# Optimization experiments

Hardware: AMD Instinct MI355X
Metric: run time of the kernel (lower is better)

Reference implementation:

```python
import jax, jax.numpy as jnp
import numpy as np

# Static configuration (matches init_kwargs)
B, C, H, W = 8, 64, 256, 256
WS = 8            # window size
HEADS = 4
DH = 16           # dim per head, HEADS*DH == C
L = WS * WS       # tokens per window
EPS_LN = 1e-5

# --- Swin relative-position index (static, numpy) ---
_coords = np.stack(np.meshgrid(np.arange(WS), np.arange(WS), indexing='ij'))  # [2,ws,ws]
_flat = _coords.reshape(2, -1)                                                # [2,L]
_rel = (_flat[:, :, None] - _flat[:, None, :]).transpose(1, 2, 0).copy()      # [L,L,2]
_rel[..., 0] += WS - 1
_rel[..., 1] += WS - 1
_rel[..., 0] *= 2 * WS - 1
REL_IDX = _rel.sum(-1)  # [L,L] ints in [0, (2ws-1)^2)


def _biasfree_ln(x, w):
    # x: [B,C,H,W]; BiasFree_LayerNorm over channel dim (biased var, no mean subtraction in scale)
    var = jnp.var(x, axis=1, keepdims=True)
    return x * jax.lax.rsqrt(var + EPS_LN) * w[None, :, None, None]


def _win_partition(t):  # [B,H,W,C] -> [N, L, C]
    t = t.reshape(B, H // WS, WS, W // WS, WS, C).transpose(0, 1, 3, 2, 4, 5)
    return t.reshape(-1, L, C)


def _win_reverse(t):  # [N, L, C] -> [B,H,W,C]
    t = t.reshape(B, H // WS, W // WS, WS, WS, C).transpose(0, 1, 3, 2, 4, 5)
    return t.reshape(B, H, W, C)


def _l2norm(t):
    # torch F.normalize(dim=-1) semantics
    n = jnp.sqrt(jnp.sum(t * t, axis=-1, keepdims=True))
    return t / jnp.maximum(n, 1e-12)


def _forward(x, illu_fea, ln1_w, ln2_w, w_qkv, b_qkv, rpb_table, w_proj, b_proj,
             temperature, w_qkv_m, w_dw, w_out_m):
    # ---------- spatial (window) attention branch ----------
    xs = _biasfree_ln(x, ln1_w).transpose(0, 2, 3, 1)          # [B,H,W,C]
    xw = _win_partition(xs)                                     # [N,L,C]
    iw = _win_partition(illu_fea.transpose(0, 2, 3, 1))         # [N,L,C]
    iw = iw.reshape(-1, L, HEADS, DH).transpose(0, 2, 1, 3)     # [N,h,L,d]

    qkv = (xw @ w_qkv + b_qkv).reshape(-1, L, 3, HEADS, DH).transpose(2, 0, 3, 1, 4)
    q, k, v = qkv[0], qkv[1], qkv[2]                            # [N,h,L,d]
    scale = DH ** (-0.5)
    attn = jnp.einsum('nhld,nhmd->nhlm', q * scale, k)          # [N,h,L,L]
    bias = rpb_table[REL_IDX.reshape(-1)].reshape(L, L, HEADS).transpose(2, 0, 1)
    attn = jax.nn.softmax(attn + bias[None], axis=-1)
    v = v * iw                                                  # illumination modulation
    out = jnp.einsum('nhlm,nhmd->nhld', attn, v)
    out = out.transpose(0, 2, 1, 3).reshape(-1, L, C) @ w_proj + b_proj
    win_out = _win_reverse(out).transpose(0, 3, 1, 2)           # [B,C,H,W]

    # ---------- channel (MDTA) attention branch ----------
    xm = _biasfree_ln(x, ln2_w)
    qkv_m = jnp.einsum('oc,bchw->bohw', w_qkv_m, xm)            # 1x1 conv, [B,3C,H,W]
    qkv_m = jax.lax.conv_general_dilated(
        qkv_m, w_dw, (1, 1), 'SAME', feature_group_count=3 * C,
        dimension_numbers=('NCHW', 'OIHW', 'NCHW'))             # depthwise 3x3
    qm, km, vm = jnp.split(qkv_m, 3, axis=1)                    # [B,C,H,W] each

    def heads(t):
        return t.reshape(B, HEADS, DH, H * W)                   # b (n d) h w -> b n d (hw)
    qm, km, vm, im = heads(qm), heads(km), heads(vm), heads(illu_fea)
    qm = _l2norm(qm)
    km = _l2norm(km)
    attn_c = jnp.einsum('bndx,bnex->bnde', qm, km) * temperature[None]  # [B,h,d,d]
    attn_c = jax.nn.softmax(attn_c, axis=-1)
    vm = vm * im                                                # illumination modulation
    out_c = jnp.einsum('bnde,bnex->bndx', attn_c, vm).reshape(B, C, H, W)
    mdta_out = jnp.einsum('oc,bchw->bohw', w_out_m, out_c)

    return x + win_out + mdta_out


def setup_inputs() -> dict:
    key = jax.random.key(0)
    ks = jax.random.split(key, 10)
    f32 = jnp.float32
    return {
        'x': jax.random.normal(ks[0], (B, C, H, W), f32),
        'illu_fea': jax.random.uniform(ks[1], (B, C, H, W), f32),
        'ln1_w': jnp.ones((C,), f32),
        'ln2_w': jnp.ones((C,), f32),
        'w_qkv': jax.random.normal(ks[2], (C, 3 * C), f32) * 0.02,
        'b_qkv': jnp.zeros((3 * C,), f32),
        'rpb_table': jax.random.normal(ks[3], ((2 * WS - 1) ** 2, HEADS), f32) * 0.02,
        'w_proj': jax.random.normal(ks[4], (C, C), f32) * 0.02,
        'b_proj': jnp.zeros((C,), f32),
        'temperature': jnp.ones((HEADS, 1, 1), f32),
        'w_qkv_m': jax.random.normal(ks[5], (3 * C, C), f32) * 0.02,
        'w_dw': jax.random.normal(ks[6], (3 * C, 1, 3, 3), f32) * 0.1,
        'w_out_m': jax.random.normal(ks[7], (C, C), f32) * 0.02,
    }


def reference(x, illu_fea, ln1_w, ln2_w, w_qkv, b_qkv, rpb_table, w_proj, b_proj,
              temperature, w_qkv_m, w_dw, w_out_m):
    return _forward(x, illu_fea, ln1_w, ln2_w, w_qkv, b_qkv, rpb_table, w_proj,
                    b_proj, temperature, w_qkv_m, w_dw, w_out_m)
```

## Files before the change

kernel.cpp:

```cpp
#include <hip/hip_runtime.h>
#include <hip/hip_bf16.h>

#define HW 65536
#define WIDTH 256
#define SP_OFF 77856768ull

typedef __attribute__((ext_vector_type(8))) short short8v;
typedef __attribute__((ext_vector_type(4))) short short4v;
typedef __attribute__((ext_vector_type(4))) float f32x4;

__device__ inline float bf2f(unsigned short u) {
  unsigned int i = ((unsigned int)u) << 16;
  float f; __builtin_memcpy(&f, &i, 4); return f;
}
__device__ inline unsigned short f2bf(float x) {
  __hip_bfloat16 h = __float2bfloat16(x);
  unsigned short u; __builtin_memcpy(&u, &h, 2); return u;
}

#define XH_IDX(p, g) ((p)*64 + ((((g) ^ ((p)&7)))<<3))
#define QC_IDX(ch, px) ((ch)*256 + ((((px)>>3) ^ ((ch)&7))<<3) + ((px)&7))
#define QCG_IDX(ch, G) ((ch)*256 + ((((G) ^ ((ch)&7)))<<3))

__device__ __forceinline__ void spatial_body(
    unsigned char* smem, int sub,
    const float* __restrict__ x, const float* __restrict__ illu,
    const float* __restrict__ ln1w, const float* __restrict__ wqkv,
    const float* __restrict__ bqkv, const float* __restrict__ rpb,
    const float* __restrict__ wproj, const float* __restrict__ bproj,
    float* __restrict__ out, unsigned short* __restrict__ sp, int use_sp)
{
  unsigned short* shbuf = (unsigned short*)smem;
  unsigned short* ks    = (unsigned short*)(smem + 18432);
  unsigned short* vs    = (unsigned short*)(smem + 27648);
  unsigned short* vsT   = (unsigned short*)(smem + 36864);
  float* rpbs           = (float*)(smem + 46080);
  float* rs_tok         = (float*)(smem + 49680);

  unsigned short* xw = shbuf;
  unsigned short* qs = shbuf + 4608;

  const int tid = threadIdx.x;
  const int b = sub & 7;
  const int grp = sub >> 3;
  const float* xb = x + (size_t)b * 64 * HW;
  const float* ib = illu + (size_t)b * 64 * HW;

  const int lane = tid & 63;
  const int w = tid >> 6;
  const int fr = lane & 15;
  const int fg = lane >> 4;
  const int hb = w * 16;

  for (int i = tid; i < 900; i += 256) rpbs[i] = rpb[i];

  short8v bfq[3][2];
  float biasr[3];
  #pragma unroll
  for (int part = 0; part < 3; ++part) {
    int o = part * 64 + hb + fr;
    biasr[part] = bqkv[o];
    #pragma unroll
    for (int kh = 0; kh < 2; ++kh)
      #pragma unroll
      for (int j = 0; j < 8; ++j) {
        int c = kh * 32 + fg * 8 + j;
        bfq[part][kh][j] = (short)f2bf(wqkv[c * 192 + o] * ln1w[c]);
      }
  }
  short8v bfp[2];
  #pragma unroll
  for (int kh = 0; kh < 2; ++kh)
    #pragma unroll
    for (int j = 0; j < 8; ++j) {
      int c = kh * 32 + fg * 8 + j;
      bfp[kh][j] = (short)f2bf(wproj[c * 64 + hb + fr]);
    }

  for (int wi = 0; wi < 4; ++wi) {
    const int win = (grp << 2) + wi;
    const int h0 = (win >> 5) << 3;
    const int w0 = (win & 31) << 3;

    for (int i = tid; i < 1024; i += 256) {
      int c = i >> 4, seg = i & 15;
      int row = seg >> 1, half = (seg & 1) * 4;
      float4 v4 = *(const float4*)&xb[(size_t)c * HW + (h0 + row) * WIDTH + w0 + half];
      int p = row * 8 + half;
      xw[(p+0)*72 + c] = f2bf(v4.x);
      xw[(p+1)*72 + c] = f2bf(v4.y);
      xw[(p+2)*72 + c] = f2bf(v4.z);
      xw[(p+3)*72 + c] = f2bf(v4.w);
    }
    __syncthreads();
    {
      int l = tid >> 2, q4 = tid & 3;
      short8v v8a = *(const short8v*)&xw[l*72 + q4*16];
      short8v v8b = *(const short8v*)&xw[l*72 + q4*16 + 8];
      float s = 0.f, s2 = 0.f;
      #pragma unroll
      for (int j = 0; j < 8; ++j) {
        float va = bf2f((unsigned short)v8a[j]), vb = bf2f((unsigned short)v8b[j]);
        s += va + vb; s2 += va * va + vb * vb;
      }
      s += __shfl_down(s, 1); s2 += __shfl_down(s2, 1);
      s += __shfl_down(s, 2); s2 += __shfl_down(s2, 2);
      if (q4 == 0) {
        float mean = s * 0.015625f;
        float var = s2 * 0.015625f - mean * mean;
        rs_tok[l] = rsqrtf(var + 1e-5f);
      }
    }
    __syncthreads();
    {
      short8v a[4][2];
      #pragma unroll
      for (int rt = 0; rt < 4; ++rt)
        #pragma unroll
        for (int kh = 0; kh < 2; ++kh)
          a[rt][kh] = *(const short8v*)&xw[(rt*16 + fr)*72 + kh*32 + fg*8];
      #pragma unroll
      for (int part = 0; part < 3; ++part) {
        float bias = biasr[part];
        #pragma unroll
        for (int rt = 0; rt < 4; ++rt) {
          f32x4 acc = {0.f, 0.f, 0.f, 0.f};
          acc = __builtin_amdgcn_mfma_f32_16x16x32_bf16(a[rt][0], bfq[part][0], acc, 0, 0, 0);
          acc = __builtin_amdgcn_mfma_f32_16x16x32_bf16(a[rt][1], bfq[part][1], acc, 0, 0, 0);
          #pragma unroll
          for (int r = 0; r < 4; ++r) {
            int t = rt*16 + fg*4 + r;
            float val = acc[r] * rs_tok[t] + bias;
            if (part == 0)      qs[t*72 + hb + fr] = f2bf(val * 0.25f);
            else if (part == 1) ks[t*72 + hb + fr] = f2bf(val);
            else                vs[t*72 + hb + fr] = f2bf(val);
          }
        }
      }
    }
    __syncthreads();
    for (int i = tid; i < 1024; i += 256) {
      int c = i >> 4, seg = i & 15;
      int row = seg >> 1, half = (seg & 1) * 4;
      float4 v4 = *(const float4*)&ib[(size_t)c * HW + (h0 + row) * WIDTH + w0 + half];
      int p = row * 8 + half;
      xw[(p+0)*72 + c] = f2bf(v4.x);
      xw[(p+1)*72 + c] = f2bf(v4.y);
      xw[(p+2)*72 + c] = f2bf(v4.z);
      xw[(p+3)*72 + c] = f2bf(v4.w);
    }
    __syncthreads();
    for (int i = tid; i < 4096; i += 256) {
      int l = i >> 6, c = i & 63;
      unsigned short vb16 = f2bf(bf2f(vs[l*72 + c]) * bf2f(xw[l*72 + c]));
      vs[l*72 + c] = vb16;
      vsT[c*72 + ((((l >> 3) ^ (c & 7)) << 3) | (l & 7))] = vb16;
    }
    __syncthreads();
    float inv_s[4];
    {
      short8v zero8 = {0,0,0,0,0,0,0,0};
      short8v kf[4], qf[4];
      #pragma unroll
      for (int t = 0; t < 4; ++t) {
        if (fg < 2) {
          kf[t] = *(const short8v*)&ks[(t*16 + fr)*72 + hb + fg*8];
          qf[t] = *(const short8v*)&qs[(t*16 + fr)*72 + hb + fg*8];
        } else { kf[t] = zero8; qf[t] = zero8; }
      }
      f32x4 st[4][4];
      #pragma unroll
      for (int kt = 0; kt < 4; ++kt)
        #pragma unroll
        for (int qt = 0; qt < 4; ++qt) {
          f32x4 z = {0.f, 0.f, 0.f, 0.f};
          st[kt][qt] = __builtin_amdgcn_mfma_f32_16x16x32_bf16(kf[kt], qf[qt], z, 0, 0, 0);
        }
      float sc[4][16];
      #pragma unroll
      for (int qt = 0; qt < 4; ++qt) {
        int qi = qt*2 + (fr >> 3);
        int qj = fr & 7;
        float mx = -1e30f;
        #pragma unroll
        for (int kt = 0; kt < 4; ++kt) {
          int ki = kt*2 + (fg >> 1);
          int kj0 = (fg & 1) * 4;
          int base = ((qi - ki + 7)*15 + (qj - kj0 + 7))*4 + w;
          #pragma unroll
          for (int r = 0; r < 4; ++r) {
            float v = st[kt][qt][r] + rpbs[base - 4*r];
            sc[qt][kt*4 + r] = v;
            mx = fmaxf(mx, v);
          }
        }
        mx = fmaxf(mx, __shfl_xor(mx, 16));
        mx = fmaxf(mx, __shfl_xor(mx, 32));
        float ss = 0.f;
        #pragma unroll
        for (int j = 0; j < 16; ++j) { float e = __expf(sc[qt][j] - mx); sc[qt][j] = e; ss += e; }
        ss += __shfl_xor(ss, 16);
        ss += __shfl_xor(ss, 32);
        inv_s[qt] = 1.f / ss;
      }
      __syncthreads();
      unsigned short* pb = shbuf + w * 2304;
      f32x4 ot[4];
      #pragma unroll
      for (int nt = 0; nt < 4; ++nt) { f32x4 z = {0.f,0.f,0.f,0.f}; ot[nt] = z; }
      #pragma unroll
      for (int P = 0; P < 2; ++P) {
        #pragma unroll
        for (int qt = 0; qt < 4; ++qt)
          #pragma unroll
          for (int k2 = 0; k2 < 2; ++k2) {
            int kt = 2*P + k2;
            unsigned int lo = (unsigned)f2bf(sc[qt][kt*4+0]) | ((unsigned)f2bf(sc[qt][kt*4+1]) << 16);
            unsigned int hi = (unsigned)f2bf(sc[qt][kt*4+2]) | ((unsigned)f2bf(sc[qt][kt*4+3]) << 16);
            uint2 pk; pk.x = lo; pk.y = hi;
            *(uint2*)&pb[(qt*16 + fr)*36 + k2*16 + fg*4] = pk;
          }
        __syncthreads();
        short8v av = *(const short8v*)&vsT[(hb + fr)*72 + (((P*4 + fg) ^ ((hb + fr) & 7)) << 3)];
        #pragma unroll
        for (int nt = 0; nt < 4; ++nt) {
          short4v p0 = *(const short4v*)&pb[(nt*16 + fr)*36 + fg*8];
          short4v p1 = *(const short4v*)&pb[(nt*16 + fr)*36 + fg*8 + 4];
          short8v bv;
          #pragma unroll
          for (int j = 0; j < 4; ++j) { bv[j] = p0[j]; bv[4+j] = p1[j]; }
          ot[nt] = __builtin_amdgcn_mfma_f32_16x16x32_bf16(av, bv, ot[nt], 0, 0, 0);
        }
        __syncthreads();
      }
      #pragma unroll
      for (int nt = 0; nt < 4; ++nt) {
        float iv = inv_s[nt];
        unsigned int lo = (unsigned)f2bf(ot[nt][0]*iv) | ((unsigned)f2bf(ot[nt][1]*iv) << 16);
        unsigned int hi = (unsigned)f2bf(ot[nt][2]*iv) | ((unsigned)f2bf(ot[nt][3]*iv) << 16);
        uint2 pk; pk.x = lo; pk.y = hi;
        *(uint2*)&ks[(nt*16 + fr)*72 + hb + fg*4] = pk;
      }
    }
    __syncthreads();
    {
      short8v a[4][2];
      #pragma unroll
      for (int rt = 0; rt < 4; ++rt)
        #pragma unroll
        for (int kh = 0; kh < 2; ++kh)
          a[rt][kh] = *(const short8v*)&ks[(rt*16 + fr)*72 + kh*32 + fg*8];
      #pragma unroll
      for (int rt = 0; rt < 4; ++rt) {
        f32x4 acc = {0.f, 0.f, 0.f, 0.f};
        acc = __builtin_amdgcn_mfma_f32_16x16x32_bf16(a[rt][0], bfp[0], acc, 0, 0, 0);
        acc = __builtin_amdgcn_mfma_f32_16x16x32_bf16(a[rt][1], bfp[1], acc, 0, 0, 0);
        #pragma unroll
        for (int r = 0; r < 4; ++r)
          vs[(rt*16 + fg*4 + r)*72 + hb + fr] = f2bf(acc[r]);
      }
    }
    __syncthreads();
    if (use_sp) {
      unsigned short* spw = sp + (size_t)(b * 1024 + win) * 4096;
      for (int i = tid; i < 1024; i += 256) {
        int row = i >> 7, rem = i & 127;
        int c = rem >> 1, half = (rem & 1) * 4;
        int p = row * 8 + half;
        size_t gofs = (size_t)c * HW + (h0 + row) * WIDTH + w0 + half;
        float4 xr4 = *(const float4*)&xb[gofs];
        float bp = bproj[c];
        unsigned int lo = (unsigned)f2bf(xr4.x + bp + bf2f(vs[(p+0)*72 + c]))
                        | ((unsigned)f2bf(xr4.y + bp + bf2f(vs[(p+1)*72 + c])) << 16);
        unsigned int hi = (unsigned)f2bf(xr4.z + bp + bf2f(vs[(p+2)*72 + c]))
                        | ((unsigned)f2bf(xr4.w + bp + bf2f(vs[(p+3)*72 + c])) << 16);
        uint2 pk; pk.x = lo; pk.y = hi;
        *(uint2*)&spw[row*512 + c*8 + half] = pk;
      }
    } else {
      for (int i = tid; i < 1024; i += 256) {
        int o = i >> 4, seg = i & 15;
        int row = seg >> 1, half = (seg & 1) * 4;
        int p = row * 8 + half;
        size_t gofs = (size_t)o * HW + (h0 + row) * WIDTH + w0 + half;
        float4 xr4 = *(const float4*)&xb[gofs];
        float bp = bproj[o];
        float4 r;
        r.x = xr4.x + bp + bf2f(vs[(p+0)*72 + o]);
        r.y = xr4.y + bp + bf2f(vs[(p+1)*72 + o]);
        r.z = xr4.z + bp + bf2f(vs[(p+2)*72 + o]);
        r.w = xr4.w + bp + bf2f(vs[(p+3)*72 + o]);
        *(float4*)&out[(size_t)b * 64 * HW + gofs] = r;
      }
    }
    __syncthreads();
  }
}

__device__ __forceinline__ void chan_body(
    unsigned char* smem, int sub,
    const float* __restrict__ x, const float* __restrict__ illu,
    const float* __restrict__ ln2w, const float* __restrict__ w1,
    const float* __restrict__ wdw,
    unsigned short* __restrict__ vm, float* __restrict__ Gp,
    float* __restrict__ Nqp, float* __restrict__ Nkp)
{
  unsigned short* xh = (unsigned short*)smem;
  unsigned short* tb = (unsigned short*)(smem + 41472);
  unsigned short* qc = (unsigned short*)(smem + 64512);
  unsigned short* kc = (unsigned short*)(smem + 72704);
  float* rsp = (float*)tb;

  const int tid = threadIdx.x;
  const int blk = ((sub & 7) << 8) | (sub >> 3);
  const int b = blk >> 8;
  const int tile = blk & 255;
  const int ty0 = (tile >> 4) << 4, tx0 = (tile & 15) << 4;
  const float* xb = x + (size_t)b * 64 * HW;

  for (int i = tid; i < 64 * 324; i += 256) {
    int c = i / 324, p = i - c * 324;
    int hy = p / 18, hx = p - hy * 18;
    int gy = ty0 + hy - 1, gx = tx0 + hx - 1;
    float v = 0.f;
    if (gy >= 0 && gy < 256 && gx >= 0 && gx < 256)
      v = xb[(size_t)c * HW + gy * WIDTH + gx];
    xh[XH_IDX(p, c >> 3) + (c & 7)] = f2bf(v);
  }
  __syncthreads();
  for (int p = tid; p < 324; p += 256) {
    float s = 0.f, s2 = 0.f;
    #pragma unroll
    for (int g = 0; g < 8; ++g) {
      short8v v8 = *(const short8v*)&xh[XH_IDX(p, g)];
      #pragma unroll
      for (int j = 0; j < 8; ++j) { float v = bf2f((unsigned short)v8[j]); s += v; s2 += v * v; }
    }
    float mean = s * 0.015625f;
    float var = s2 * 0.015625f - mean * mean;
    rsp[p] = rsqrtf(var + 1e-5f);
  }
  __syncthreads();
  for (int i = tid; i < 2592; i += 256) {
    int p = i >> 3;
    float rs = rsp[p];
    short8v v8 = *(const short8v*)&xh[i * 8];
    #pragma unroll
    for (int j = 0; j < 8; ++j) v8[j] = (short)f2bf(bf2f((unsigned short)v8[j]) * rs);
    *(short8v*)&xh[i * 8] = v8;
  }
  __syncthreads();

  const int lane = tid & 63;
  const int wid = tid >> 6;
  const int fcol = lane & 15;
  const int fk = lane >> 4;
  const int dpy = (tid >> 2) & 15;
  const int dg = tid & 3;

  auto gemm32 = [&](int qb, int kb) {
    short8v bq[2], bk[2];
    const float* wrq = w1 + (size_t)(qb + fcol) * 64;
    const float* wrk = w1 + (size_t)(kb + fcol) * 64;
    #pragma unroll
    for (int s = 0; s < 2; ++s) {
      int cs = fk * 8 + s * 32;
      #pragma unroll
      for (int j = 0; j < 8; ++j) {
        float lw = ln2w[cs + j];
        bq[s][j] = (short)f2bf(wrq[cs + j] * lw);
        bk[s][j] = (short)f2bf(wrk[cs + j] * lw);
      }
    }
    for (int t = wid; t < 21; t += 4) {
      int ar = t * 16 + fcol;
      short8v a0, a1;
      if (ar < 324) {
        a0 = *(const short8v*)&xh[XH_IDX(ar, fk)];
        a1 = *(const short8v*)&xh[XH_IDX(ar, fk + 4)];
      } else {
        short8v z = {0,0,0,0,0,0,0,0};
        a0 = z; a1 = z;
      }
      f32x4 aq = {0.f, 0.f, 0.f, 0.f};
      f32x4 ak = {0.f, 0.f, 0.f, 0.f};
      aq = __builtin_amdgcn_mfma_f32_16x16x32_bf16(a0, bq[0], aq, 0, 0, 0);
      aq = __builtin_amdgcn_mfma_f32_16x16x32_bf16(a1, bq[1], aq, 0, 0, 0);
      ak = __builtin_amdgcn_mfma_f32_16x16x32_bf16(a0, bk[0], ak, 0, 0, 0);
      ak = __builtin_amdgcn_mfma_f32_16x16x32_bf16(a1, bk[1], ak, 0, 0, 0);
      #pragma unroll
      for (int r = 0; r < 4; ++r) {
        int px = t * 16 + fk * 4 + r;
        if (px < 324) {
          int hy = px / 18, hx = px - hy * 18;
          tb[fcol * 360 + hy * 20 + hx]        = f2bf(aq[r]);
          tb[(16 + fcol) * 360 + hy * 20 + hx] = f2bf(ak[r]);
        }
      }
    }
  };

  float dout8[8][4];
  auto dw32 = [&](int qwb, int kwb) {
    #pragma unroll
    for (int oc8 = 0; oc8 < 8; ++oc8) {
      int oc = wid * 8 + oc8;
      int ch = (oc < 16) ? (qwb + oc) : (kwb + oc - 16);
      const float* w9 = wdw + (size_t)ch * 9;
      float wk[9];
      #pragma unroll
      for (int t = 0; t < 9; ++t) wk[t] = w9[t];
      float a0 = 0.f, a1 = 0.f, a2 = 0.f, a3 = 0.f;
      #pragma unroll
      for (int ky = 0; ky < 3; ++ky) {
        int base = oc * 360 + (dpy + ky) * 20 + dg * 4;
        short4v t4 = *(const short4v*)&tb[base];
        unsigned int t2 = *(const unsigned int*)&tb[base + 4];
        float e0 = bf2f((unsigned short)t4[0]);
        float e1 = bf2f((unsigned short)t4[1]);
        float e2 = bf2f((unsigned short)t4[2]);
        float e3 = bf2f((unsigned short)t4[3]);
        float e4 = bf2f((unsigned short)(t2 & 0xffff));
        float e5 = bf2f((unsigned short)(t2 >> 16));
        float k0 = wk[ky*3+0], k1 = wk[ky*3+1], k2 = wk[ky*3+2];
        a0 += k0*e0 + k1*e1 + k2*e2;
        a1 += k0*e1 + k1*e2 + k2*e3;
        a2 += k0*e2 + k1*e3 + k2*e4;
        a3 += k0*e3 + k1*e4 + k2*e5;
      }
      dout8[oc8][0] = a0; dout8[oc8][1] = a1;
      dout8[oc8][2] = a2; dout8[oc8][3] = a3;
    }
  };

  for (int n = 0; n < 4; ++n) {
    gemm32(16 * n, 64 + 16 * n);
    __syncthreads();
    dw32(16 * n, 64 + 16 * n);
    #pragma unroll
    for (int oc8 = 0; oc8 < 8; ++oc8) {
      int oc = wid * 8 + oc8;
      unsigned short* dst = (oc < 16) ? qc : kc;
      int row = oc & 15;
      #pragma unroll
      for (int i = 0; i < 4; ++i)
        dst[QC_IDX(row, dpy*16 + dg*4 + i)] = f2bf(dout8[oc8][i]);
    }
    __syncthreads();
    {
      int ch = tid >> 4, seg = tid & 15;
      float sq = 0.f, sk = 0.f;
      #pragma unroll
      for (int j = 0; j < 16; ++j) {
        float vq = bf2f(qc[QC_IDX(ch, seg * 16 + j)]); sq += vq * vq;
        float vk = bf2f(kc[QC_IDX(ch, seg * 16 + j)]); sk += vk * vk;
      }
      sq += __shfl_xor(sq, 1); sq += __shfl_xor(sq, 2); sq += __shfl_xor(sq, 4); sq += __shfl_xor(sq, 8);
      sk += __shfl_xor(sk, 1); sk += __shfl_xor(sk, 2); sk += __shfl_xor(sk, 4); sk += __shfl_xor(sk, 8);
      if (seg == 0) {
        Nqp[(size_t)blk * 64 + n * 16 + ch] = sq;
        Nkp[(size_t)blk * 64 + n * 16 + ch] = sk;
      }
    }
    if (wid == 0) {
      f32x4 g = {0.f, 0.f, 0.f, 0.f};
      #pragma unroll
      for (int s = 0; s < 8; ++s) {
        int G = fk + 4 * s;
        short8v aq = *(const short8v*)&qc[QCG_IDX(fcol, G)];
        short8v bk = *(const short8v*)&kc[QCG_IDX(fcol, G)];
        g = __builtin_amdgcn_mfma_f32_16x16x32_bf16(aq, bk, g, 0, 0, 0);
      }
      float* gp = Gp + ((size_t)blk * 4 + n) * 256;
      #pragma unroll
      for (int r = 0; r < 4; ++r) gp[(fk * 4 + r) * 16 + fcol] = g[r];
    }
  }
  const float* ib = illu + (size_t)b * 64 * HW;
  for (int j = 0; j < 2; ++j) {
    gemm32(128 + 32 * j, 144 + 32 * j);
    __syncthreads();
    dw32(128 + 32 * j, 144 + 32 * j);
    int gy = ty0 + dpy, gx = tx0 + dg * 4;
    size_t ppos = (size_t)gy * WIDTH + gx;
    #pragma unroll
    for (int oc8 = 0; oc8 < 8; ++oc8) {
      int vc = 32 * j + wid * 8 + oc8;
      float4 iv4 = *(const float4*)&ib[(size_t)vc * HW + ppos];
      unsigned int lo = (unsigned)f2bf(dout8[oc8][0] * iv4.x)
                      | ((unsigned)f2bf(dout8[oc8][1] * iv4.y) << 16);
      unsigned int hi = (unsigned)f2bf(dout8[oc8][2] * iv4.z)
                      | ((unsigned)f2bf(dout8[oc8][3] * iv4.w) << 16);
      uint2 pk; pk.x = lo; pk.y = hi;
      *(uint2*)&vm[((size_t)b * 64 + vc) * HW + ppos] = pk;
    }
    __syncthreads();
  }
}

__global__ __launch_bounds__(256, 2) void k_fused(
    const float* __restrict__ x, const float* __restrict__ illu,
    const float* __restrict__ ln1w, const float* __restrict__ ln2w,
    const float* __restrict__ wqkv, const float* __restrict__ bqkv,
    const float* __restrict__ rpb, const float* __restrict__ wproj,
    const float* __restrict__ bproj, const float* __restrict__ w1,
    const float* __restrict__ wdw,
    float* __restrict__ out, unsigned short* __restrict__ sp, int use_sp,
    unsigned short* __restrict__ vm, float* __restrict__ Gp,
    float* __restrict__ Nqp, float* __restrict__ Nkp)
{
  __shared__ __align__(16) unsigned char smem[80896];
  const int sub = blockIdx.x >> 1;
  if (blockIdx.x & 1)
    chan_body(smem, sub, x, illu, ln2w, w1, wdw, vm, Gp, Nqp, Nkp);
  else
    spatial_body(smem, sub, x, illu, ln1w, wqkv, bqkv, rpb, wproj, bproj, out, sp, use_sp);
}

__global__ __launch_bounds__(256) void k_reduce1(
    const float* __restrict__ Gp, const float* __restrict__ Nqp, const float* __restrict__ Nkp,
    float* __restrict__ G2, float* __restrict__ Nq2, float* __restrict__ Nk2)
{
  const int blk = blockIdx.x;
  const int b = blk >> 5, g = blk & 31;
  const int tid = threadIdx.x;
  float ga[4] = {0.f, 0.f, 0.f, 0.f};
  for (int t = 0; t < 8; ++t) {
    const float* src = Gp + ((size_t)(b * 256 + g * 8 + t)) * 1024;
    #pragma unroll
    for (int j = 0; j < 4; ++j) ga[j] += src[tid + j * 256];
  }
  float* dst = G2 + ((size_t)(b * 32 + g)) * 1024;
  #pragma unroll
  for (int j = 0; j < 4; ++j) dst[tid + j * 256] = ga[j];
  if (tid < 128) {
    int ch = tid & 63; bool isq = tid < 64;
    const float* np = isq ? Nqp : Nkp;
    float s = 0.f;
    for (int t = 0; t < 8; ++t) s += np[((size_t)(b * 256 + g * 8 + t)) * 64 + ch];
    (isq ? Nq2 : Nk2)[(size_t)(b * 32 + g) * 64 + ch] = s;
  }
}

__global__ __launch_bounds__(256) void k_reduce2(
    const float* __restrict__ G2, const float* __restrict__ Nq2, const float* __restrict__ Nk2,
    const float* __restrict__ temp, const float* __restrict__ wout, float* __restrict__ M)
{
  __shared__ float Gs[1024];
  __shared__ float As[4][16][17];
  __shared__ float nq[64], nk[64];
  const int b = blockIdx.x;
  const int tid = threadIdx.x;
  float ga[4] = {0.f, 0.f, 0.f, 0.f};
  for (int g = 0; g < 32; ++g) {
    const float* src = G2 + ((size_t)(b * 32 + g)) * 1024;
    #pragma unroll
    for (int j = 0; j < 4; ++j) ga[j] += src[tid + j * 256];
  }
  #pragma unroll
  for (int j = 0; j < 4; ++j) Gs[tid + j * 256] = ga[j];
  if (tid < 128) {
    int ch = tid & 63; bool isq = tid < 64;
    const float* n2 = isq ? Nq2 : Nk2;
    float s = 0.f;
    for (int g = 0; g < 32; ++g) s += n2[(size_t)(b * 32 + g) * 64 + ch];
    float r = fmaxf(sqrtf(s), 1e-12f);
    (isq ? nq : nk)[ch] = r;
  }
  __syncthreads();
  if (tid < 64) {
    int n = tid >> 4, d = tid & 15;
    float tv = temp[n];
    float row[16]; float mx = -1e30f;
    #pragma unroll
    for (int e = 0; e < 16; ++e) {
      float v = Gs[n * 256 + d * 16 + e] / (nq[n * 16 + d] * nk[n * 16 + e]) * tv;
      row[e] = v; mx = fmaxf(mx, v);
    }
    float s = 0.f;
    #pragma unroll
    for (int e = 0; e < 16; ++e) { float ev = __expf(row[e] - mx); row[e] = ev; s += ev; }
    float inv = 1.f / s;
    #pragma unroll
    for (int e = 0; e < 16; ++e) As[n][d][e] = row[e] * inv;
  }
  __syncthreads();
  float* Mb = M + (size_t)b * 4096;
  for (int i = tid; i < 4096; i += 256) {
    int o = i >> 6, cp = i & 63;
    int n = cp >> 4, e = cp & 15;
    float a = 0.f;
    #pragma unroll
    for (int d = 0; d < 16; ++d) a += wout[o * 64 + n * 16 + d] * As[n][d][e];
    Mb[i] = a;
  }
}

__global__ __launch_bounds__(256, 3) void k_mdta_out(
    const unsigned short* __restrict__ vm, const float* __restrict__ M,
    const unsigned short* __restrict__ sp, int use_sp,
    float* __restrict__ out)
{
  __shared__ __align__(16) float Ml[4096];
  __shared__ __align__(16) unsigned short spl[64 * 264];
  const int blk = blockIdx.x;
  const int b = blk >> 8;
  const int y = blk & 255;
  const int tid = threadIdx.x;

  const float* Mb = M + (size_t)b * 4096;
  for (int i = tid; i < 4096; i += 256) Ml[i] = Mb[i];
  if (use_sp) {
    int wy = y >> 3, py = y & 7;
    const unsigned short* spb = sp + ((((size_t)b * 1024 + wy * 32) * 8) + py) * 512;
    for (int k = 0; k < 8; ++k) {
      int i3 = k * 256 + tid;
      int o = i3 & 63, wx = i3 >> 6;
      short8v v8 = *(const short8v*)&spb[(size_t)wx * 4096 + o * 8];
      *(short8v*)&spl[o * 264 + wx * 8] = v8;
    }
  }
  __syncthreads();
  float xcol[64];
  const unsigned short* vb = vm + (size_t)b * 64 * HW + y * 256 + tid;
  #pragma unroll
  for (int c = 0; c < 64; ++c) xcol[c] = bf2f(vb[(size_t)c * HW]);
  float* ob = out + (size_t)b * 64 * HW + y * 256 + tid;
  for (int o = 0; o < 64; ++o) {
    const float4* mr = (const float4*)&Ml[o * 64];
    float acc = 0.f;
    #pragma unroll
    for (int g = 0; g < 16; ++g) {
      float4 m4 = mr[g];
      acc += m4.x * xcol[g*4] + m4.y * xcol[g*4+1] + m4.z * xcol[g*4+2] + m4.w * xcol[g*4+3];
    }
    if (use_sp) ob[(size_t)o * HW] = bf2f(spl[o * 264 + tid]) + acc;
    else        ob[(size_t)o * HW] += acc;
  }
}

extern "C" void kernel_launch(void* const* d_in, const int* in_sizes, int n_in,
                              void* d_out, int out_size, void* d_ws, size_t ws_size,
                              hipStream_t stream) {
  const float* x     = (const float*)d_in[0];
  const float* illu  = (const float*)d_in[1];
  const float* ln1w  = (const float*)d_in[2];
  const float* ln2w  = (const float*)d_in[3];
  const float* wqkv  = (const float*)d_in[4];
  const float* bqkv  = (const float*)d_in[5];
  const float* rpb   = (const float*)d_in[6];
  const float* wproj = (const float*)d_in[7];
  const float* bproj = (const float*)d_in[8];
  const float* temp  = (const float*)d_in[9];
  const float* w1    = (const float*)d_in[10];
  const float* wdw   = (const float*)d_in[11];
  const float* wout  = (const float*)d_in[12];
  float* out = (float*)d_out;

  char* ws = (char*)d_ws;
  unsigned short* vm = (unsigned short*)ws;
  float* Gp  = (float*)(ws + 67108864);
  float* Nqp = (float*)(ws + 75497472);
  float* Nkp = (float*)(ws + 76021760);
  float* G2  = (float*)(ws + 76546048);
  float* Nq2 = (float*)(ws + 77594624);
  float* Nk2 = (float*)(ws + 77660160);
  float* M   = (float*)(ws + 77725696);
  unsigned short* sp = (unsigned short*)(ws + SP_OFF);
  int use_sp = (ws_size >= SP_OFF + 67108864ull) ? 1 : 0;

  k_fused<<<4096, 256, 0, stream>>>(x, illu, ln1w, ln2w, wqkv, bqkv, rpb, wproj, bproj,
                                    w1, wdw, out, sp, use_sp, vm, Gp, Nqp, Nkp);
  k_reduce1<<<256, 256, 0, stream>>>(Gp, Nqp, Nkp, G2, Nq2, Nk2);
  k_reduce2<<<8, 256, 0, stream>>>(G2, Nq2, Nk2, temp, wout, M);
  k_mdta_out<<<2048, 256, 0, stream>>>(vm, M, sp, use_sp, out);
}
```

Before: 655.6 us.

## Precompute expanded bf16 relative-position bias in LDS and remap blocks per XCD

Replaces the per-element indexed lookup into the 900-entry fp32 relative-position table with a dense per-head [64x68] bf16 bias matrix built once per block in shared memory, so the softmax loop reads contiguous short4 vectors instead of computing scattered indices. The bias matrix overlaps the former vsT and rs_tok regions, and rs_tok is moved to reuse that space. Block IDs are also remapped so each batch image goes to one XCD (blockIdx & 7), keeping its data local to that XCD's L2. The cost is a 16K-element bias build per block and bf16 rounding of the bias values.

```diff
diff --git a/kernel.cpp b/kernel.cpp
--- a/kernel.cpp
+++ b/kernel.cpp
@@ -23,7 +23,7 @@
 #define QCG_IDX(ch, G) ((ch)*256 + ((((G) ^ ((ch)&7)))<<3))
 
 __device__ __forceinline__ void spatial_body(
-    unsigned char* smem, int sub,
+    unsigned char* smem, int b, int grp,
     const float* __restrict__ x, const float* __restrict__ illu,
     const float* __restrict__ ln1w, const float* __restrict__ wqkv,
     const float* __restrict__ bqkv, const float* __restrict__ rpb,
@@ -34,15 +34,13 @@
   unsigned short* ks    = (unsigned short*)(smem + 18432);
   unsigned short* vs    = (unsigned short*)(smem + 27648);
   unsigned short* vsT   = (unsigned short*)(smem + 36864);
-  float* rpbs           = (float*)(smem + 46080);
-  float* rs_tok         = (float*)(smem + 49680);
+  float* rs_tok         = (float*)(smem + 36864);
+  unsigned short* biasx = (unsigned short*)(smem + 46080);
 
   unsigned short* xw = shbuf;
   unsigned short* qs = shbuf + 4608;
 
   const int tid = threadIdx.x;
-  const int b = sub & 7;
-  const int grp = sub >> 3;
   const float* xb = x + (size_t)b * 64 * HW;
   const float* ib = illu + (size_t)b * 64 * HW;
 
@@ -52,7 +50,11 @@
   const int fg = lane >> 4;
   const int hb = w * 16;
 
-  for (int i = tid; i < 900; i += 256) rpbs[i] = rpb[i];
+  for (int i = tid; i < 16384; i += 256) {
+    int w4 = i >> 12, q = (i >> 6) & 63, k = i & 63;
+    int ridx = ((q >> 3) - (k >> 3) + 7) * 15 + ((q & 7) - (k & 7) + 7);
+    biasx[(w4 * 64 + q) * 68 + k] = f2bf(rpb[ridx * 4 + w4]);
+  }
 
   short8v bfq[3][2];
   float biasr[3];
@@ -179,17 +181,14 @@
       float sc[4][16];
       #pragma unroll
       for (int qt = 0; qt < 4; ++qt) {
-        int qi = qt*2 + (fr >> 3);
-        int qj = fr & 7;
+        const unsigned short* brow = &biasx[(w * 64 + qt * 16 + fr) * 68];
         float mx = -1e30f;
         #pragma unroll
         for (int kt = 0; kt < 4; ++kt) {
-          int ki = kt*2 + (fg >> 1);
-          int kj0 = (fg & 1) * 4;
-          int base = ((qi - ki + 7)*15 + (qj - kj0 + 7))*4 + w;
+          short4v b4 = *(const short4v*)&brow[kt * 16 + fg * 4];
           #pragma unroll
           for (int r = 0; r < 4; ++r) {
-            float v = st[kt][qt][r] + rpbs[base - 4*r];
+            float v = st[kt][qt][r] + bf2f((unsigned short)b4[r]);
             sc[qt][kt*4 + r] = v;
             mx = fmaxf(mx, v);
           }
@@ -298,7 +297,7 @@
 }
 
 __device__ __forceinline__ void chan_body(
-    unsigned char* smem, int sub,
+    unsigned char* smem, int b, int tile,
     const float* __restrict__ x, const float* __restrict__ illu,
     const float* __restrict__ ln2w, const float* __restrict__ w1,
     const float* __restrict__ wdw,
@@ -312,9 +311,7 @@
   float* rsp = (float*)tb;
 
   const int tid = threadIdx.x;
-  const int blk = ((sub & 7) << 8) | (sub >> 3);
-  const int b = blk >> 8;
-  const int tile = blk & 255;
+  const int blk = (b << 8) | tile;
   const int ty0 = (tile >> 4) << 4, tx0 = (tile & 15) << 4;
   const float* xb = x + (size_t)b * 64 * HW;
 
@@ -510,11 +507,13 @@
     float* __restrict__ Nqp, float* __restrict__ Nkp)
 {
   __shared__ __align__(16) unsigned char smem[80896];
-  const int sub = blockIdx.x >> 1;
-  if (blockIdx.x & 1)
-    chan_body(smem, sub, x, illu, ln2w, w1, wdw, vm, Gp, Nqp, Nkp);
+  const int xcd = blockIdx.x & 7;
+  const int j = blockIdx.x >> 3;
+  const int idx = j >> 1;
+  if (j & 1)
+    chan_body(smem, xcd, idx, x, illu, ln2w, w1, wdw, vm, Gp, Nqp, Nkp);
   else
-    spatial_body(smem, sub, x, illu, ln1w, wqkv, bqkv, rpb, wproj, bproj, out, sp, use_sp);
+    spatial_body(smem, xcd, idx, x, illu, ln1w, wqkv, bqkv, rpb, wproj, bproj, out, sp, use_sp);
 }
 
 __global__ __launch_bounds__(256) void k_reduce1(
```

After: 645.8 us (median of 3 runs). About the same (-1.5%).
